# Performance work log

Measured on AMD Instinct MI355X. Metric: run time of the kernel, lower is better.

## Reference

```python
import jax, jax.numpy as jnp
import numpy as np

HEADS = 32
N_KV_HEADS = 8
HEAD_DIM = 128        # n_embd // heads
N_EMBD = 4096
B, T = 2, 2048


def setup_inputs() -> dict:
    key = jax.random.key(0)
    ks = jax.random.split(key, 8)
    x = jax.random.normal(ks[0], (B, T, N_EMBD), jnp.float32)
    # Llama RoPE frequencies: theta = 10000^(-2i/d), angle = pos * theta
    pos = jnp.arange(T, dtype=jnp.float32)
    inv_freq = 1.0 / (10000.0 ** (jnp.arange(0, HEAD_DIM, 2, dtype=jnp.float32) / HEAD_DIM))
    ang = pos[:, None] * inv_freq[None, :]                      # (T, HEAD_DIM//2)
    freq_cos = jnp.cos(ang)
    freq_sin = jnp.sin(ang)
    s = 0.02
    w_q_w = jax.random.normal(ks[1], (HEADS * HEAD_DIM, N_EMBD), jnp.float32) * s
    w_q_b = jax.random.normal(ks[2], (HEADS * HEAD_DIM,), jnp.float32) * s
    w_kv_w = jax.random.normal(ks[3], (2 * N_KV_HEADS * HEAD_DIM, N_EMBD), jnp.float32) * s
    w_kv_b = jax.random.normal(ks[4], (2 * N_KV_HEADS * HEAD_DIM,), jnp.float32) * s
    proj_w = jax.random.normal(ks[5], (N_EMBD, N_EMBD), jnp.float32) * s
    proj_b = jax.random.normal(ks[6], (N_EMBD,), jnp.float32) * s
    return {"x": x, "freq_cos": freq_cos, "freq_sin": freq_sin,
            "w_q_w": w_q_w, "w_q_b": w_q_b, "w_kv_w": w_kv_w, "w_kv_b": w_kv_b,
            "proj_w": proj_w, "proj_b": proj_b, "start_pos": 0}


def _rope(t, cos, sin):
    # t: (B, H, T, HEAD_DIM); complex multiply on interleaved (even, odd) pairs
    tr = t.reshape(t.shape[:-1] + (HEAD_DIM // 2, 2))
    t0, t1 = tr[..., 0], tr[..., 1]
    r0 = t0 * cos - t1 * sin
    r1 = t0 * sin + t1 * cos
    return jnp.stack([r0, r1], axis=-1).reshape(t.shape)


def reference(x, freq_cos, freq_sin, w_q_w, w_q_b, w_kv_w, w_kv_b, proj_w, proj_b, start_pos):
    Bx, Tx, C = x.shape
    g = HEADS // N_KV_HEADS  # GQA group size
    q = (x @ w_q_w.T + w_q_b).reshape(Bx, Tx, HEADS, HEAD_DIM).transpose(0, 2, 1, 3)
    kv = x @ w_kv_w.T + w_kv_b
    k, v = jnp.split(kv, 2, axis=-1)
    k = k.reshape(Bx, Tx, N_KV_HEADS, HEAD_DIM).transpose(0, 2, 1, 3)
    v = v.reshape(Bx, Tx, N_KV_HEADS, HEAD_DIM).transpose(0, 2, 1, 3)
    cos = freq_cos[:Tx]  # (T, HEAD_DIM//2), broadcasts over (B, H)
    sin = freq_sin[:Tx]
    q = _rope(q, cos, sin)
    k = _rope(k, cos, sin)
    # GQA without materializing repeated KV: group query heads per KV head
    qg = q.reshape(Bx, N_KV_HEADS, g, Tx, HEAD_DIM)
    scores = jnp.einsum('bkgqd,bkld->bkgql', qg, k) / jnp.sqrt(jnp.float32(HEAD_DIM))
    causal = jnp.tril(jnp.ones((Tx, Tx), dtype=bool))
    scores = jnp.where(causal, scores, -jnp.inf)
    p = jax.nn.softmax(scores, axis=-1)
    y = jnp.einsum('bkgql,bkld->bkgqd', p, v)
    y = y.reshape(Bx, HEADS, Tx, HEAD_DIM).transpose(0, 2, 1, 3).reshape(Bx, Tx, C)
    return y @ proj_w.T + proj_b
```

## Files before the change

kernel.cpp:

```cpp
#include <hip/hip_runtime.h>
#include <hip/hip_bf16.h>
#include <stdint.h>

typedef __hip_bfloat16 bf16;
typedef __attribute__((ext_vector_type(8))) __bf16 bf16x8;
typedef __attribute__((ext_vector_type(4))) float f32x4;
typedef __attribute__((ext_vector_type(16))) float f32x16;

__device__ __forceinline__ void gld16(void* lds, const void* g) {
  __builtin_amdgcn_global_load_lds(
      (const __attribute__((address_space(1))) void*)(uintptr_t)(g),
      (__attribute__((address_space(3))) void*)(uint32_t)(uintptr_t)(lds),
      16, 0, 0);
}

__device__ __forceinline__ uint16_t f2bf(float f) {
  union { bf16 h; uint16_t u; } x; x.h = __float2bfloat16(f); return x.u;
}
__device__ __forceinline__ float bf2f(uint16_t v) {
  union { uint32_t u; float f; } x; x.u = ((uint32_t)v) << 16; return x.f;
}
__device__ __forceinline__ uint32_t pk2(float lo, float hi) {
  uint32_t r;
  asm("v_cvt_pk_bf16_f32 %0, %1, %2" : "=v"(r) : "v"(lo), "v"(hi));
  return r;
}

__global__ __launch_bounds__(256) void k_cast(const float4* __restrict__ in,
                                              uint2* __restrict__ out, int n4) {
  int i = blockIdx.x * 256 + threadIdx.x;
  if (i >= n4) return;
  float4 v = in[i];
  uint32_t a = ((uint32_t)f2bf(v.y) << 16) | f2bf(v.x);
  uint32_t b = ((uint32_t)f2bf(v.w) << 16) | f2bf(v.z);
  out[i] = make_uint2(a, b);
}

template <int OUT_BF16>
__global__ __launch_bounds__(512, 2) void k_gemm256(
    const bf16* __restrict__ A, const bf16* __restrict__ B,
    const float* __restrict__ bias, void* __restrict__ C,
    int M, int N, int K, int gx) {
  __shared__ __align__(16) char lds[131072];
  const int tid = threadIdx.x;
  const int lane = tid & 63;
  const int w = tid >> 6;
  const int wm = w >> 2;
  const int wn = w & 3;
  const int lm = lane & 15;
  const int lg = lane >> 4;

  const int nwg = gridDim.x;
  const int cpx = nwg >> 3;
  const int bid0 = blockIdx.x;
  const int bid = (bid0 & 7) * cpx + (bid0 >> 3);
  const int bx = bid % gx;
  const int by = bid / gx;
  const size_t bm = (size_t)by * 256;
  const size_t bn = (size_t)bx * 256;

  const int srow = tid >> 3;
  const int scb = ((tid & 7) * 16) ^ ((srow & 7) << 4);
  const char* asrc[4];
  const char* bsrc[4];
#pragma unroll
  for (int j = 0; j < 4; ++j) {
    asrc[j] = (const char*)(A + (bm + j * 64 + srow) * K) + scb;
    bsrc[j] = (const char*)(B + (bn + j * 64 + srow) * K) + scb;
  }
  const int ldst = tid * 16;

  const int colb0 = (lg * 16) ^ ((lm & 7) << 4);
  const int colb1 = colb0 ^ 64;

  f32x4 acc[8][4];
#pragma unroll
  for (int i = 0; i < 8; ++i)
#pragma unroll
    for (int j = 0; j < 4; ++j) acc[i][j] = (f32x4){0.f, 0.f, 0.f, 0.f};

  const int NT = K >> 6;

  {
    char* la = lds;
    char* lb = lds + 32768;
#pragma unroll
    for (int j = 0; j < 4; ++j) {
      gld16(la + j * 8192 + ldst, asrc[j]);
      gld16(lb + j * 8192 + ldst, bsrc[j]);
    }
  }
  __syncthreads();

  for (int t = 0; t < NT; ++t) {
    const int slot = t & 1;
    const char* la = lds + slot * 65536;
    const char* lb = la + 32768;

    bf16x8 bfrag[4][2];
#pragma unroll
    for (int ni = 0; ni < 4; ++ni) {
      const int br = wn * 64 + ni * 16 + lm;
      bfrag[ni][0] = *(const bf16x8*)(lb + br * 128 + colb0);
      bfrag[ni][1] = *(const bf16x8*)(lb + br * 128 + colb1);
    }
    bf16x8 af[2][2];
#pragma unroll
    for (int q = 0; q < 2; ++q) {
      const int ar = wm * 128 + q * 16 + lm;
      af[q][0] = *(const bf16x8*)(la + ar * 128 + colb0);
      af[q][1] = *(const bf16x8*)(la + ar * 128 + colb1);
    }

    if (t + 1 < NT) {
      char* na = lds + (slot ^ 1) * 65536;
      char* nb = na + 32768;
      const size_t ko = (size_t)(t + 1) * 128;
#pragma unroll
      for (int j = 0; j < 4; ++j) {
        gld16(na + j * 8192 + ldst, asrc[j] + ko);
        gld16(nb + j * 8192 + ldst, bsrc[j] + ko);
      }
    }

#pragma unroll
    for (int p = 0; p < 4; ++p) {
      asm volatile("s_waitcnt lgkmcnt(0)" ::: "memory");
      __builtin_amdgcn_sched_barrier(0);
      __builtin_amdgcn_s_setprio(1);
      bf16x8 a00 = af[0][0], a01 = af[0][1];
      bf16x8 a10 = af[1][0], a11 = af[1][1];
#pragma unroll
      for (int ni = 0; ni < 4; ++ni) {
        acc[2 * p][ni] = __builtin_amdgcn_mfma_f32_16x16x32_bf16(
            a00, bfrag[ni][0], acc[2 * p][ni], 0, 0, 0);
        acc[2 * p][ni] = __builtin_amdgcn_mfma_f32_16x16x32_bf16(
            a01, bfrag[ni][1], acc[2 * p][ni], 0, 0, 0);
        acc[2 * p + 1][ni] = __builtin_amdgcn_mfma_f32_16x16x32_bf16(
            a10, bfrag[ni][0], acc[2 * p + 1][ni], 0, 0, 0);
        acc[2 * p + 1][ni] = __builtin_amdgcn_mfma_f32_16x16x32_bf16(
            a11, bfrag[ni][1], acc[2 * p + 1][ni], 0, 0, 0);
      }
      __builtin_amdgcn_s_setprio(0);
      if (p < 3) {
#pragma unroll
        for (int q = 0; q < 2; ++q) {
          const int ar = wm * 128 + (2 * (p + 1) + q) * 16 + lm;
          af[q][0] = *(const bf16x8*)(la + ar * 128 + colb0);
          af[q][1] = *(const bf16x8*)(la + ar * 128 + colb1);
        }
      }
    }
    __syncthreads();
  }

#pragma unroll
  for (int ni = 0; ni < 4; ++ni) {
    const size_t col = bn + wn * 64 + ni * 16 + lm;
    const float bv = bias[col];
#pragma unroll
    for (int mi = 0; mi < 8; ++mi) {
#pragma unroll
      for (int r = 0; r < 4; ++r) {
        const size_t row = bm + wm * 128 + mi * 16 + lg * 4 + r;
        const float v = acc[mi][ni][r] + bv;
        if (OUT_BF16)
          ((bf16*)C)[row * N + col] = __float2bfloat16(v);
        else
          ((float*)C)[row * N + col] = v;
      }
    }
  }
}

__global__ __launch_bounds__(256) void k_rope_q(
    const uint32_t* __restrict__ qin, const float* __restrict__ fc,
    const float* __restrict__ fs, uint32_t* __restrict__ qout) {
  const int tid = blockIdx.x * 256 + threadIdx.x;
  const int i = tid & 63;
  const int h = (tid >> 6) & 31;
  const int t = (tid >> 11) & 2047;
  const int b = tid >> 22;
  const uint32_t u = qin[tid];
  const float t0 = bf2f((uint16_t)(u & 0xffff));
  const float t1 = bf2f((uint16_t)(u >> 16));
  const float c = fc[t * 64 + i];
  const float s = fs[t * 64 + i];
  const float r0 = t0 * c - t1 * s;
  const float r1 = t0 * s + t1 * c;
  const uint32_t o = ((uint32_t)f2bf(r1) << 16) | f2bf(r0);
  qout[(((size_t)(b * 32 + h)) * 2048 + t) * 64 + i] = o;
}

__global__ __launch_bounds__(256) void k_rope_k(
    const uint32_t* __restrict__ kvin, const float* __restrict__ fc,
    const float* __restrict__ fs, uint32_t* __restrict__ kout) {
  const int tid = blockIdx.x * 256 + threadIdx.x;
  const int i = tid & 63;
  const int kvh = (tid >> 6) & 7;
  const int t = (tid >> 9) & 2047;
  const int b = tid >> 20;
  const uint32_t u = kvin[((size_t)(b * 2048 + t)) * 1024 + kvh * 64 + i];
  const float t0 = bf2f((uint16_t)(u & 0xffff));
  const float t1 = bf2f((uint16_t)(u >> 16));
  const float c = fc[t * 64 + i];
  const float s = fs[t * 64 + i];
  const float r0 = t0 * c - t1 * s;
  const float r1 = t0 * s + t1 * c;
  const uint32_t o = ((uint32_t)f2bf(r1) << 16) | f2bf(r0);
  kout[(((size_t)(b * 8 + kvh)) * 2048 + t) * 64 + i] = o;
}

__global__ __launch_bounds__(256) void k_vt(const bf16* __restrict__ kv,
                                            bf16* __restrict__ vt) {
  __shared__ __align__(16) bf16 tile[64][130];
  const int bh = blockIdx.y;
  const int b = bh >> 3, kvh = bh & 7;
  const int t0 = blockIdx.x * 64;
  const int tid = threadIdx.x;
  const int d0 = (tid & 15) * 8;
  const int tr = tid >> 4;
#pragma unroll
  for (int j = 0; j < 4; ++j) {
    const int trow = tr + j * 16;
    const bf16* src =
        kv + ((size_t)(b * 2048) + t0 + trow) * 2048 + 1024 + kvh * 128 + d0;
    uint4 v = *(const uint4*)src;
    uint32_t* dst = (uint32_t*)&tile[trow][d0];
    dst[0] = v.x; dst[1] = v.y; dst[2] = v.z; dst[3] = v.w;
  }
  __syncthreads();
  const int d = tid >> 1;
  const int th = (tid & 1) * 32;
  uint4* out = (uint4*)(vt + (((size_t)bh) * 128 + d) * 2048 + t0 + th);
  union { bf16 h; uint16_t u; } cv;
#pragma unroll
  for (int j = 0; j < 4; ++j) {
    uint32_t wds[4];
#pragma unroll
    for (int p = 0; p < 4; ++p) {
      cv.h = tile[th + j * 8 + p * 2][d];
      uint32_t lo = cv.u;
      cv.h = tile[th + j * 8 + p * 2 + 1][d];
      wds[p] = lo | ((uint32_t)cv.u << 16);
    }
    uint4 val; val.x = wds[0]; val.y = wds[1]; val.z = wds[2]; val.w = wds[3];
    out[j] = val;
  }
}

__global__ __launch_bounds__(512) void k_attn(
    const bf16* __restrict__ Q, const bf16* __restrict__ Kr,
    const bf16* __restrict__ Vt, bf16* __restrict__ Y) {
  constexpr int T = 2048;
  __shared__ __align__(16) char lds[65536];
  const int tid = threadIdx.x;
  const int lane = tid & 63;
  const int w = tid >> 6;
  const int l31 = lane & 31;
  const int hi = lane >> 5;

  const int n = blockIdx.x;
  const int qc = 7 - (n >> 6);
  const int bh = n & 63;
  const int b = bh >> 5, h = bh & 31, kvh = h >> 2;

  const int qrow = qc * 256 + w * 32 + l31;
  const int qmaxw = qc * 256 + w * 32 + 31;
  const int NT = qc * 4 + 4;

  const bf16* qptr = Q + (((size_t)(b * 32 + h)) * T + qrow) * 128 + hi * 8;
  bf16x8 qf[8];
#pragma unroll
  for (int kt = 0; kt < 8; ++kt) qf[kt] = *(const bf16x8*)(qptr + kt * 16);

  const char* kg = (const char*)(Kr + ((size_t)(b * 8 + kvh)) * T * 128);
  const char* vg = (const char*)(Vt + ((size_t)(b * 8 + kvh)) * 128 * T);
  const char* ksrc[2];
  const char* vsrc[2];
  int kdst[2], vdst[2];
#pragma unroll
  for (int j = 0; j < 2; ++j) {
    const int o = j * 8192 + tid * 16;
    const int krow = o >> 8, kin = o & 255;
    ksrc[j] = kg + (size_t)krow * 256 + (kin ^ ((krow & 15) << 4));
    kdst[j] = o;
    const int vrow = o >> 7, vin = o & 127;
    vsrc[j] = vg + (size_t)vrow * (T * 2) + (vin ^ ((vrow & 7) << 4));
    vdst[j] = 16384 + o;
  }

  f32x16 oacc[4];
#pragma unroll
  for (int d = 0; d < 4; ++d)
#pragma unroll
    for (int r = 0; r < 16; ++r) oacc[d][r] = 0.f;
  float m = -1e30f, l = 0.f;
  const float c1 = 0.08838834764831845f * 1.44269504089f;

#pragma unroll
  for (int j = 0; j < 2; ++j) {
    gld16(lds + kdst[j], ksrc[j]);
    gld16(lds + vdst[j], vsrc[j]);
  }

  for (int it = 0; it < NT; ++it) {
    const int buf = it & 1;
    __syncthreads();

    if (it + 1 < NT) {
      const int nb = buf ^ 1;
      const size_t ko = (size_t)(it + 1) * 16384;
      const size_t vo = (size_t)(it + 1) * 128;
#pragma unroll
      for (int j = 0; j < 2; ++j) {
        gld16(lds + nb * 32768 + kdst[j], ksrc[j] + ko);
        gld16(lds + nb * 32768 + vdst[j], vsrc[j] + vo);
      }
    }

    const int kt0 = it * 64;
    if (kt0 <= qmaxw) {
      const char* kb = lds + buf * 32768;
      const char* vb = kb + 16384;

      f32x16 s0, s1;
#pragma unroll
      for (int r = 0; r < 16; ++r) { s0[r] = 0.f; s1[r] = 0.f; }
      const int kswz = (l31 & 15) << 4;
#pragma unroll
      for (int kt = 0; kt < 8; ++kt) {
        const int cb = (kt * 32 + hi * 16) ^ kswz;
        bf16x8 kf0 = *(const bf16x8*)(kb + l31 * 256 + cb);
        bf16x8 kf1 = *(const bf16x8*)(kb + (32 + l31) * 256 + cb);
        s0 = __builtin_amdgcn_mfma_f32_32x32x16_bf16(kf0, qf[kt], s0, 0, 0, 0);
        s1 = __builtin_amdgcn_mfma_f32_32x32x16_bf16(kf1, qf[kt], s1, 0, 0, 0);
      }

      float tmax = -1e30f;
#pragma unroll
      for (int r = 0; r < 16; ++r) {
        const int key0 = kt0 + (r & 3) + 8 * (r >> 2) + 4 * hi;
        float v0 = s0[r] * c1;
        v0 = (key0 <= qrow) ? v0 : -1e30f;
        s0[r] = v0; tmax = fmaxf(tmax, v0);
        float v1 = s1[r] * c1;
        v1 = (key0 + 32 <= qrow) ? v1 : -1e30f;
        s1[r] = v1; tmax = fmaxf(tmax, v1);
      }
      tmax = fmaxf(tmax, __shfl_xor(tmax, 32));

      const float mn = fmaxf(m, tmax);
      const float alpha = __builtin_amdgcn_exp2f(m - mn);
      m = mn;
      l *= alpha;
      float aw[16];
#pragma unroll
      for (int g = 0; g < 4; ++g)
#pragma unroll
        for (int c = 0; c < 4; ++c)
          aw[g * 4 + c] = __shfl(alpha, g * 8 + hi * 4 + c, 64);
#pragma unroll
      for (int r = 0; r < 16; ++r) {
        const float a2 = aw[(r >> 2) * 4 + (r & 3)];
        oacc[0][r] *= a2; oacc[1][r] *= a2;
        oacc[2][r] *= a2; oacc[3][r] *= a2;
      }

      float ls = 0.f;
#pragma unroll
      for (int r = 0; r < 16; ++r) {
        const float p0 = __builtin_amdgcn_exp2f(s0[r] - m); s0[r] = p0; ls += p0;
        const float p1 = __builtin_amdgcn_exp2f(s1[r] - m); s1[r] = p1; ls += p1;
      }
      l += ls + __shfl_xor(ls, 32);

#pragma unroll
      for (int t = 0; t < 4; ++t) {
        uint32_t a0, a1, b0, b1;
        if (t == 0) {
          a0 = pk2(s0[0], s0[1]); a1 = pk2(s0[2], s0[3]);
          b0 = pk2(s0[4], s0[5]); b1 = pk2(s0[6], s0[7]);
        } else if (t == 1) {
          a0 = pk2(s0[8], s0[9]); a1 = pk2(s0[10], s0[11]);
          b0 = pk2(s0[12], s0[13]); b1 = pk2(s0[14], s0[15]);
        } else if (t == 2) {
          a0 = pk2(s1[0], s1[1]); a1 = pk2(s1[2], s1[3]);
          b0 = pk2(s1[4], s1[5]); b1 = pk2(s1[6], s1[7]);
        } else {
          a0 = pk2(s1[8], s1[9]); a1 = pk2(s1[10], s1[11]);
          b0 = pk2(s1[12], s1[13]); b1 = pk2(s1[14], s1[15]);
        }
        const uint32_t sa0 = __shfl_xor(a0, 32), sa1 = __shfl_xor(a1, 32);
        const uint32_t sb0 = __shfl_xor(b0, 32), sb1 = __shfl_xor(b1, 32);
        union { uint32_t u[4]; bf16x8 v; } A;
        A.u[0] = hi ? sb0 : a0;
        A.u[1] = hi ? sb1 : a1;
        A.u[2] = hi ? b0 : sa0;
        A.u[3] = hi ? b1 : sa1;
#pragma unroll
        for (int d = 0; d < 4; ++d) {
          const int vrow = d * 32 + l31;
          const int vcb = (32 * t + 16 * hi) ^ ((vrow & 7) << 4);
          bf16x8 vf = *(const bf16x8*)(vb + vrow * 128 + vcb);
          oacc[d] = __builtin_amdgcn_mfma_f32_32x32x16_bf16(A.v, vf, oacc[d], 0, 0, 0);
        }
      }
    }
    __syncthreads();
  }

  const float linv = 1.0f / l;
  float lw[16];
#pragma unroll
  for (int g = 0; g < 4; ++g)
#pragma unroll
    for (int c = 0; c < 4; ++c)
      lw[g * 4 + c] = __shfl(linv, g * 8 + hi * 4 + c, 64);
  bf16* yb = Y + ((size_t)b * T) * 4096 + h * 128 + l31;
#pragma unroll
  for (int d = 0; d < 4; ++d)
#pragma unroll
    for (int r = 0; r < 16; ++r) {
      const int qp = (r & 3) + 8 * (r >> 2) + 4 * hi;
      const size_t trow = qc * 256 + w * 32 + qp;
      yb[trow * 4096 + d * 32] =
          __float2bfloat16(oacc[d][r] * lw[(r >> 2) * 4 + (r & 3)]);
    }
}

extern "C" void kernel_launch(void* const* d_in, const int* in_sizes, int n_in,
                              void* d_out, int out_size, void* d_ws, size_t ws_size,
                              hipStream_t stream) {
  const float* x = (const float*)d_in[0];
  const float* fcos = (const float*)d_in[1];
  const float* fsin = (const float*)d_in[2];
  const float* wq = (const float*)d_in[3];
  const float* bq = (const float*)d_in[4];
  const float* wkv = (const float*)d_in[5];
  const float* bkv = (const float*)d_in[6];
  const float* wp = (const float*)d_in[7];
  const float* bp = (const float*)d_in[8];

  char* ws = (char*)d_ws;
  size_t off = 0;
  auto alloc = [&](size_t bytes) {
    char* p = ws + off;
    off += (bytes + 255) & ~(size_t)255;
    return p;
  };
  bf16* xb = (bf16*)alloc(16777216ull * 2);
  bf16* wqb = (bf16*)alloc(16777216ull * 2);
  bf16* wkvb = (bf16*)alloc(8388608ull * 2);
  bf16* wpb = (bf16*)alloc(16777216ull * 2);
  bf16* qb = (bf16*)alloc(16777216ull * 2);
  bf16* kvb = (bf16*)alloc(8388608ull * 2);
  bf16* qr = (bf16*)alloc(16777216ull * 2);
  bf16* kr = (bf16*)alloc(4194304ull * 2);
  bf16* vt = (bf16*)alloc(4194304ull * 2);
  bf16* yb = qb;

  k_cast<<<16384, 256, 0, stream>>>((const float4*)x, (uint2*)xb, 4194304);
  k_cast<<<16384, 256, 0, stream>>>((const float4*)wq, (uint2*)wqb, 4194304);
  k_cast<<<8192, 256, 0, stream>>>((const float4*)wkv, (uint2*)wkvb, 2097152);
  k_cast<<<16384, 256, 0, stream>>>((const float4*)wp, (uint2*)wpb, 4194304);

  k_gemm256<1><<<256, 512, 0, stream>>>(xb, wqb, bq, qb, 4096, 4096, 4096, 16);
  k_gemm256<1><<<128, 512, 0, stream>>>(xb, wkvb, bkv, kvb, 4096, 2048, 4096, 8);

  k_rope_q<<<32768, 256, 0, stream>>>((const uint32_t*)qb, fcos, fsin, (uint32_t*)qr);
  k_rope_k<<<8192, 256, 0, stream>>>((const uint32_t*)kvb, fcos, fsin, (uint32_t*)kr);
  k_vt<<<dim3(32, 16), 256, 0, stream>>>(kvb, vt);

  k_attn<<<512, 512, 0, stream>>>(qr, kr, vt, yb);

  k_gemm256<0><<<256, 512, 0, stream>>>(yb, wpb, bp, d_out, 4096, 4096, 4096, 16);
}
```

Before: 525.7 us.

## Fuse Q and KV projections into one GEMM and double-buffer A fragments

```diff
diff --git a/kernel.cpp b/kernel.cpp
--- a/kernel.cpp
+++ b/kernel.cpp
@@ -34,6 +34,13 @@
   uint32_t a = ((uint32_t)f2bf(v.y) << 16) | f2bf(v.x);
   uint32_t b = ((uint32_t)f2bf(v.w) << 16) | f2bf(v.z);
   out[i] = make_uint2(a, b);
+}
+
+__global__ __launch_bounds__(256) void k_bcat(const float* __restrict__ bq,
+                                              const float* __restrict__ bkv,
+                                              float* __restrict__ o) {
+  const int i = blockIdx.x * 256 + threadIdx.x;
+  o[i] = (i < 4096) ? bq[i] : bkv[i - 4096];
 }
 
 template <int OUT_BF16>
@@ -104,12 +111,12 @@
       bfrag[ni][0] = *(const bf16x8*)(lb + br * 128 + colb0);
       bfrag[ni][1] = *(const bf16x8*)(lb + br * 128 + colb1);
     }
-    bf16x8 af[2][2];
+    bf16x8 afA[2][2], afB[2][2];
 #pragma unroll
     for (int q = 0; q < 2; ++q) {
       const int ar = wm * 128 + q * 16 + lm;
-      af[q][0] = *(const bf16x8*)(la + ar * 128 + colb0);
-      af[q][1] = *(const bf16x8*)(la + ar * 128 + colb1);
+      afA[q][0] = *(const bf16x8*)(la + ar * 128 + colb0);
+      afA[q][1] = *(const bf16x8*)(la + ar * 128 + colb1);
     }
 
     if (t + 1 < NT) {
@@ -125,11 +132,23 @@
 
 #pragma unroll
     for (int p = 0; p < 4; ++p) {
-      asm volatile("s_waitcnt lgkmcnt(0)" ::: "memory");
+      auto& cur = (p & 1) ? afB : afA;
+      auto& nxt = (p & 1) ? afA : afB;
+      if (p < 3) {
+#pragma unroll
+        for (int q = 0; q < 2; ++q) {
+          const int ar = wm * 128 + (2 * (p + 1) + q) * 16 + lm;
+          nxt[q][0] = *(const bf16x8*)(la + ar * 128 + colb0);
+          nxt[q][1] = *(const bf16x8*)(la + ar * 128 + colb1);
+        }
+        asm volatile("s_waitcnt lgkmcnt(4)" ::: "memory");
+      } else {
+        asm volatile("s_waitcnt lgkmcnt(0)" ::: "memory");
+      }
       __builtin_amdgcn_sched_barrier(0);
       __builtin_amdgcn_s_setprio(1);
-      bf16x8 a00 = af[0][0], a01 = af[0][1];
-      bf16x8 a10 = af[1][0], a11 = af[1][1];
+      bf16x8 a00 = cur[0][0], a01 = cur[0][1];
+      bf16x8 a10 = cur[1][0], a11 = cur[1][1];
 #pragma unroll
       for (int ni = 0; ni < 4; ++ni) {
         acc[2 * p][ni] = __builtin_amdgcn_mfma_f32_16x16x32_bf16(
@@ -142,14 +161,6 @@
             a11, bfrag[ni][1], acc[2 * p + 1][ni], 0, 0, 0);
       }
       __builtin_amdgcn_s_setprio(0);
-      if (p < 3) {
-#pragma unroll
-        for (int q = 0; q < 2; ++q) {
-          const int ar = wm * 128 + (2 * (p + 1) + q) * 16 + lm;
-          af[q][0] = *(const bf16x8*)(la + ar * 128 + colb0);
-          af[q][1] = *(const bf16x8*)(la + ar * 128 + colb1);
-        }
-      }
     }
     __syncthreads();
   }
@@ -174,14 +185,14 @@
 }
 
 __global__ __launch_bounds__(256) void k_rope_q(
-    const uint32_t* __restrict__ qin, const float* __restrict__ fc,
+    const uint32_t* __restrict__ qkv, const float* __restrict__ fc,
     const float* __restrict__ fs, uint32_t* __restrict__ qout) {
   const int tid = blockIdx.x * 256 + threadIdx.x;
   const int i = tid & 63;
   const int h = (tid >> 6) & 31;
   const int t = (tid >> 11) & 2047;
   const int b = tid >> 22;
-  const uint32_t u = qin[tid];
+  const uint32_t u = qkv[((size_t)(b * 2048 + t)) * 3072 + h * 64 + i];
   const float t0 = bf2f((uint16_t)(u & 0xffff));
   const float t1 = bf2f((uint16_t)(u >> 16));
   const float c = fc[t * 64 + i];
@@ -193,14 +204,15 @@
 }
 
 __global__ __launch_bounds__(256) void k_rope_k(
-    const uint32_t* __restrict__ kvin, const float* __restrict__ fc,
+    const uint32_t* __restrict__ qkv, const float* __restrict__ fc,
     const float* __restrict__ fs, uint32_t* __restrict__ kout) {
   const int tid = blockIdx.x * 256 + threadIdx.x;
   const int i = tid & 63;
   const int kvh = (tid >> 6) & 7;
   const int t = (tid >> 9) & 2047;
   const int b = tid >> 20;
-  const uint32_t u = kvin[((size_t)(b * 2048 + t)) * 1024 + kvh * 64 + i];
+  const uint32_t u =
+      qkv[((size_t)(b * 2048 + t)) * 3072 + 2048 + kvh * 64 + i];
   const float t0 = bf2f((uint16_t)(u & 0xffff));
   const float t1 = bf2f((uint16_t)(u >> 16));
   const float c = fc[t * 64 + i];
@@ -211,7 +223,7 @@
   kout[(((size_t)(b * 8 + kvh)) * 2048 + t) * 64 + i] = o;
 }
 
-__global__ __launch_bounds__(256) void k_vt(const bf16* __restrict__ kv,
+__global__ __launch_bounds__(256) void k_vt(const bf16* __restrict__ qkv,
                                             bf16* __restrict__ vt) {
   __shared__ __align__(16) bf16 tile[64][130];
   const int bh = blockIdx.y;
@@ -224,7 +236,7 @@
   for (int j = 0; j < 4; ++j) {
     const int trow = tr + j * 16;
     const bf16* src =
-        kv + ((size_t)(b * 2048) + t0 + trow) * 2048 + 1024 + kvh * 128 + d0;
+        qkv + ((size_t)(b * 2048) + t0 + trow) * 6144 + 5120 + kvh * 128 + d0;
     uint4 v = *(const uint4*)src;
     uint32_t* dst = (uint32_t*)&tile[trow][d0];
     dst[0] = v.x; dst[1] = v.y; dst[2] = v.z; dst[3] = v.w;
@@ -453,24 +465,24 @@
   bf16* wqb = (bf16*)alloc(16777216ull * 2);
   bf16* wkvb = (bf16*)alloc(8388608ull * 2);
   bf16* wpb = (bf16*)alloc(16777216ull * 2);
-  bf16* qb = (bf16*)alloc(16777216ull * 2);
-  bf16* kvb = (bf16*)alloc(8388608ull * 2);
+  bf16* qkv = (bf16*)alloc(25165824ull * 2);
   bf16* qr = (bf16*)alloc(16777216ull * 2);
   bf16* kr = (bf16*)alloc(4194304ull * 2);
   bf16* vt = (bf16*)alloc(4194304ull * 2);
-  bf16* yb = qb;
+  float* bqkv = (float*)alloc(6144ull * 4);
+  bf16* yb = qkv;
 
   k_cast<<<16384, 256, 0, stream>>>((const float4*)x, (uint2*)xb, 4194304);
   k_cast<<<16384, 256, 0, stream>>>((const float4*)wq, (uint2*)wqb, 4194304);
   k_cast<<<8192, 256, 0, stream>>>((const float4*)wkv, (uint2*)wkvb, 2097152);
   k_cast<<<16384, 256, 0, stream>>>((const float4*)wp, (uint2*)wpb, 4194304);
-
-  k_gemm256<1><<<256, 512, 0, stream>>>(xb, wqb, bq, qb, 4096, 4096, 4096, 16);
-  k_gemm256<1><<<128, 512, 0, stream>>>(xb, wkvb, bkv, kvb, 4096, 2048, 4096, 8);
-
-  k_rope_q<<<32768, 256, 0, stream>>>((const uint32_t*)qb, fcos, fsin, (uint32_t*)qr);
-  k_rope_k<<<8192, 256, 0, stream>>>((const uint32_t*)kvb, fcos, fsin, (uint32_t*)kr);
-  k_vt<<<dim3(32, 16), 256, 0, stream>>>(kvb, vt);
+  k_bcat<<<24, 256, 0, stream>>>(bq, bkv, bqkv);
+
+  k_gemm256<1><<<384, 512, 0, stream>>>(xb, wqb, bqkv, qkv, 4096, 6144, 4096, 24);
+
+  k_rope_q<<<32768, 256, 0, stream>>>((const uint32_t*)qkv, fcos, fsin, (uint32_t*)qr);
+  k_rope_k<<<8192, 256, 0, stream>>>((const uint32_t*)qkv, fcos, fsin, (uint32_t*)kr);
+  k_vt<<<dim3(32, 16), 256, 0, stream>>>(qkv, vt);
 
   k_attn<<<512, 512, 0, stream>>>(qr, kr, vt, yb);
 
```

New measurement: 517.0 us. No clear change (-1.6%).
